# Optimization experiments

Hardware: AMD Instinct MI355X
Metric: run time of the kernel (lower is better)

## Reference

```python
import jax, jax.numpy as jnp
import numpy as np

B, T, C, H = 8, 2048, 1024, 128  # batch, seq (=block_size), n_embd, head_size


def setup_inputs() -> dict:
    key = jax.random.key(0)
    kx, kk, kq, kv = jax.random.split(key, 4)
    x = jax.random.normal(kx, (B, T, C), dtype=jnp.float32)
    # nn.Linear(n_embd, head_size, bias=False) weights, stored as (in, out) for x @ W
    s = 1.0 / np.sqrt(C)
    Wk = jax.random.normal(kk, (C, H), dtype=jnp.float32) * s
    Wq = jax.random.normal(kq, (C, H), dtype=jnp.float32) * s
    Wv = jax.random.normal(kv, (C, H), dtype=jnp.float32) * s
    return {"x": x, "Wk": Wk, "Wq": Wq, "Wv": Wv}


def reference(x, Wk, Wq, Wv):
    # x: [B, T, C]
    Bx, Tx, Cx = x.shape
    k = x @ Wk  # [B, T, H]
    q = x @ Wq  # [B, T, H]
    v = x @ Wv  # [B, T, H]
    # NOTE: source multiplies by C**0.5 (not 1/sqrt), kept faithfully
    wei = jnp.einsum("bth,bsh->bts", q, k) * (Cx ** 0.5)  # [B, T, T]
    causal = jnp.tril(jnp.ones((Tx, Tx), dtype=bool))
    wei = jnp.where(causal, wei, -jnp.inf)
    wei = jax.nn.softmax(wei, axis=-1)
    # dropout omitted (eval-mode reference)
    return wei @ v  # [B, T, H]
```

## Files before the change

### kernel.cpp

```cpp
#include <hip/hip_runtime.h>

constexpr int kB = 8;
constexpr int kT = 2048;
constexpr int kC = 1024;
constexpr int kH = 128;
constexpr int kM = kB * kT;
constexpr size_t kMH = (size_t)kM * kH;
constexpr size_t kWH = (size_t)kC * kH;

#define QSCALE 46.166241308446828f

typedef __attribute__((ext_vector_type(8))) short bf16x8;
typedef __attribute__((ext_vector_type(4))) float f32x4;


__device__ inline unsigned short f2bf_rne(float f) {
    union { float f; unsigned int u; } x; x.f = f;
    unsigned int r = x.u + 0x7fff + ((x.u >> 16) & 1);
    return (unsigned short)(r >> 16);
}
__device__ inline float bf2f(unsigned short h) {
    union { float f; unsigned int u; } x; x.u = ((unsigned int)h) << 16;
    return x.f;
}
__device__ inline unsigned int pack_hi2(float a, float b) {
    return __builtin_amdgcn_perm(__float_as_uint(b), __float_as_uint(a),
                                 0x07060302u);
}
__device__ inline float hi_part(float v) {
    return __uint_as_float(__float_as_uint(v) & 0xffff0000u);
}
__device__ inline void load_lds16(const unsigned short* g, unsigned short* l) {
    __builtin_amdgcn_global_load_lds(
        (const __attribute__((address_space(1))) unsigned int*)g,
        (__attribute__((address_space(3))) unsigned int*)l, 16, 0, 0);
}

template <int CTRL>
__device__ inline float dpp_rot(float x) {
    return __int_as_float(__builtin_amdgcn_update_dpp(
        0, __float_as_int(x), CTRL, 0xf, 0xf, false));
}
__device__ inline float rowmax16(float x) {
    x = fmaxf(x, dpp_rot<0x121>(x));
    x = fmaxf(x, dpp_rot<0x122>(x));
    x = fmaxf(x, dpp_rot<0x124>(x));
    x = fmaxf(x, dpp_rot<0x128>(x));
    return x;
}
__device__ inline float rowsum16(float x) {
    x += dpp_rot<0x121>(x);
    x += dpp_rot<0x122>(x);
    x += dpp_rot<0x124>(x);
    x += dpp_rot<0x128>(x);
    return x;
}

__global__ __launch_bounds__(256) void prep_w(
    const float* __restrict__ Wk, const float* __restrict__ Wq,
    const float* __restrict__ Wv, unsigned short* __restrict__ ws)
{
    const int h = blockIdx.x;
    const int mat = blockIdx.y;
    const float* W = (mat == 0) ? Wq : (mat == 1) ? Wk : Wv;
    unsigned short* hi = ws + 5 * kMH + (size_t)(mat * 2) * kWH;
    unsigned short* lo = hi + kWH;

    const int k0 = threadIdx.x * 4;
    unsigned short hv[4], lv[4];
#pragma unroll
    for (int j = 0; j < 4; ++j) {
        const float f = W[(size_t)(k0 + j) * kH + h];
        hv[j] = f2bf_rne(f);
        lv[j] = f2bf_rne(f - bf2f(hv[j]));
    }
    *(uint2*)&hi[(size_t)h * kC + k0] =
        make_uint2(((unsigned)hv[1] << 16) | hv[0], ((unsigned)hv[3] << 16) | hv[2]);
    *(uint2*)&lo[(size_t)h * kC + k0] =
        make_uint2(((unsigned)lv[1] << 16) | lv[0], ((unsigned)lv[3] << 16) | lv[2]);
}

__global__ __launch_bounds__(256) void qkv_mfma(
    const float* __restrict__ x, unsigned short* __restrict__ ws)
{
    __shared__ __align__(16) unsigned short Bh[128 * 64];
    __shared__ __align__(16) unsigned short Bl[128 * 64];

    const int idx = blockIdx.x;
    const int mat = idx >> 8;
    const int m0 = (idx & 255) * 64;
    const unsigned short* wThi = ws + 5 * kMH + (size_t)(mat * 2) * kWH;
    const unsigned short* wTlo = wThi + kWH;

    const int tid = threadIdx.x;
    const int w = tid >> 6, lane = tid & 63;
    const int li = lane & 15, quad = lane >> 4;

    const float* xrow = x + (size_t)(m0 + w * 16 + li) * kC;

    f32x4 acc[8];
#pragma unroll
    for (int j = 0; j < 8; ++j) acc[j] = (f32x4){0.f, 0.f, 0.f, 0.f};

    for (int kt = 0; kt < kC; kt += 64) {
        if (kt) __syncthreads();
#pragma unroll
        for (int u = 0; u < 4; ++u) {
            const int f = u * 256 + tid;
            const int row = f >> 3, g = (f & 7) ^ (row & 7);
            load_lds16(wThi + (size_t)row * kC + kt + g * 8, Bh + f * 8);
            if (mat <= 1)
                load_lds16(wTlo + (size_t)row * kC + kt + g * 8, Bl + f * 8);
        }
        float4 xa[2][2];
#pragma unroll
        for (int kc = 0; kc < 2; ++kc) {
            xa[kc][0] = *(const float4*)(xrow + kt + kc * 32 + quad * 8);
            xa[kc][1] = *(const float4*)(xrow + kt + kc * 32 + quad * 8 + 4);
        }
        bf16x8 ah[2], al[2];
        if (mat <= 1) {
#pragma unroll
            for (int kc = 0; kc < 2; ++kc) {
                const float4 a0 = xa[kc][0], a1 = xa[kc][1];
                unsigned int hp[4], lp[4];
                hp[0] = pack_hi2(a0.x, a0.y); hp[1] = pack_hi2(a0.z, a0.w);
                hp[2] = pack_hi2(a1.x, a1.y); hp[3] = pack_hi2(a1.z, a1.w);
                lp[0] = pack_hi2(a0.x - hi_part(a0.x), a0.y - hi_part(a0.y));
                lp[1] = pack_hi2(a0.z - hi_part(a0.z), a0.w - hi_part(a0.w));
                lp[2] = pack_hi2(a1.x - hi_part(a1.x), a1.y - hi_part(a1.y));
                lp[3] = pack_hi2(a1.z - hi_part(a1.z), a1.w - hi_part(a1.w));
                ah[kc] = *(bf16x8*)hp;
                al[kc] = *(bf16x8*)lp;
            }
        } else {
#pragma unroll
            for (int kc = 0; kc < 2; ++kc) {
                const float4 a0 = xa[kc][0], a1 = xa[kc][1];
                unsigned short e[8];
                e[0] = f2bf_rne(a0.x); e[1] = f2bf_rne(a0.y);
                e[2] = f2bf_rne(a0.z); e[3] = f2bf_rne(a0.w);
                e[4] = f2bf_rne(a1.x); e[5] = f2bf_rne(a1.y);
                e[6] = f2bf_rne(a1.z); e[7] = f2bf_rne(a1.w);
                ah[kc] = *(bf16x8*)e;
            }
        }
        __syncthreads();

        if (mat <= 1) {
#pragma unroll
            for (int kc = 0; kc < 2; ++kc)
#pragma unroll
                for (int nt = 0; nt < 8; ++nt) {
                    const int row = nt * 16 + li;
                    const int pos = (kc * 4 + quad) ^ (row & 7);
                    const bf16x8 bh = *(const bf16x8*)&Bh[row * 64 + pos * 8];
                    const bf16x8 bl = *(const bf16x8*)&Bl[row * 64 + pos * 8];
                    acc[nt] = __builtin_amdgcn_mfma_f32_16x16x32_bf16(ah[kc], bh, acc[nt], 0, 0, 0);
                    acc[nt] = __builtin_amdgcn_mfma_f32_16x16x32_bf16(al[kc], bh, acc[nt], 0, 0, 0);
                    acc[nt] = __builtin_amdgcn_mfma_f32_16x16x32_bf16(ah[kc], bl, acc[nt], 0, 0, 0);
                }
        } else {
#pragma unroll
            for (int kc = 0; kc < 2; ++kc)
#pragma unroll
                for (int nt = 0; nt < 8; ++nt) {
                    const int row = nt * 16 + li;
                    const int pos = (kc * 4 + quad) ^ (row & 7);
                    const bf16x8 bh = *(const bf16x8*)&Bh[row * 64 + pos * 8];
                    acc[nt] = __builtin_amdgcn_mfma_f32_16x16x32_bf16(ah[kc], bh, acc[nt], 0, 0, 0);
                }
        }
    }

    if (mat <= 1) {
        unsigned short* hip_ = ws + (size_t)(mat * 2) * kMH;
        unsigned short* lop  = hip_ + kMH;
        const float sc = (mat == 0) ? QSCALE : 1.0f;
#pragma unroll
        for (int nt = 0; nt < 8; ++nt) {
            const int col = nt * 16 + li;
#pragma unroll
            for (int reg = 0; reg < 4; ++reg) {
                const int row = m0 + w * 16 + quad * 4 + reg;
                const float v = acc[nt][reg] * sc;
                hip_[(size_t)row * kH + col] = (unsigned short)(__float_as_uint(v) >> 16);
                lop[(size_t)row * kH + col] =
                    (unsigned short)(__float_as_uint(v - hi_part(v)) >> 16);
            }
        }
    } else {
        unsigned short* vt = ws + 4 * kMH;
        const int bb = m0 >> 11;
        const int t0 = (m0 & (kT - 1)) + w * 16 + quad * 4;
#pragma unroll
        for (int nt = 0; nt < 8; ++nt) {
            const int h = nt * 16 + li;
            ushort4 pk;
            pk.x = f2bf_rne(acc[nt][0]);
            pk.y = f2bf_rne(acc[nt][1]);
            pk.z = f2bf_rne(acc[nt][2]);
            pk.w = f2bf_rne(acc[nt][3]);
            *(ushort4*)&vt[((size_t)(bb * kH + h)) * kT + t0] = pk;
        }
    }
}

__global__ __launch_bounds__(256, 2) void attn_mfma(
    const unsigned short* __restrict__ ws, float* __restrict__ out)
{
    __shared__ __align__(16) unsigned short Ps[4][2][16][40];
    __shared__ __align__(16) float Ml[4][32][2];
    __shared__ __align__(16) float Obuf[3][32][128];

    const int tid = threadIdx.x;
    const int w = tid >> 6, lane = tid & 63;
    const int li = lane & 15, quad = lane >> 4;

    const int idx = blockIdx.x;
    const int b = idx & 7;
    const int j = idx >> 3;
    const int qt = (j < 32) ? j : 95 - j;
    const int i0 = qt * 32;
    const int nc = qt + 1;

    const unsigned short* qhi = ws;
    const unsigned short* qlo = ws + kMH;
    const unsigned short* khi = ws + 2 * kMH;
    const unsigned short* klo = ws + 3 * kMH;
    const unsigned short* vt  = ws + 4 * kMH;

    bf16x8 qh[2][4], ql[2][4];
#pragma unroll
    for (int mi = 0; mi < 2; ++mi) {
        const size_t qoff = ((size_t)(b * kT + i0 + mi * 16 + li)) * kH;
#pragma unroll
        for (int kc = 0; kc < 4; ++kc) {
            qh[mi][kc] = *(const bf16x8*)(qhi + qoff + kc * 32 + quad * 8);
            ql[mi][kc] = *(const bf16x8*)(qlo + qoff + kc * 32 + quad * 8);
        }
    }

    f32x4 o[2][8];
#pragma unroll
    for (int mi = 0; mi < 2; ++mi)
#pragma unroll
        for (int ht = 0; ht < 8; ++ht) o[mi][ht] = (f32x4){0.f, 0.f, 0.f, 0.f};
    float m_i[2][4], l_i[2][4];
#pragma unroll
    for (int mi = 0; mi < 2; ++mi)
#pragma unroll
        for (int reg = 0; reg < 4; ++reg) { m_i[mi][reg] = -3.0e38f; l_i[mi][reg] = 0.f; }

    for (int jc = w; jc < nc; jc += 4) {
        const int t0 = jc * 32;
        bf16x8 vf[8];
#pragma unroll
        for (int ht = 0; ht < 8; ++ht)
            vf[ht] = *(const bf16x8*)(vt + (size_t)(b * kH + ht * 16 + li) * kT +
                                      t0 + quad * 8);
        f32x4 s[2][2];
#pragma unroll
        for (int mi = 0; mi < 2; ++mi)
#pragma unroll
            for (int nt = 0; nt < 2; ++nt) s[mi][nt] = (f32x4){0.f, 0.f, 0.f, 0.f};
#pragma unroll
        for (int kc = 0; kc < 4; ++kc) {
            bf16x8 kh[2], kl[2];
#pragma unroll
            for (int nt = 0; nt < 2; ++nt) {
                const size_t ka =
                    ((size_t)(b * kT + t0 + nt * 16 + li)) * kH + kc * 32 + quad * 8;
                kh[nt] = *(const bf16x8*)(khi + ka);
                kl[nt] = *(const bf16x8*)(klo + ka);
            }
#pragma unroll
            for (int mi = 0; mi < 2; ++mi)
#pragma unroll
                for (int nt = 0; nt < 2; ++nt) {
                    s[mi][nt] = __builtin_amdgcn_mfma_f32_16x16x32_bf16(qh[mi][kc], kh[nt], s[mi][nt], 0, 0, 0);
                    s[mi][nt] = __builtin_amdgcn_mfma_f32_16x16x32_bf16(ql[mi][kc], kh[nt], s[mi][nt], 0, 0, 0);
                    s[mi][nt] = __builtin_amdgcn_mfma_f32_16x16x32_bf16(qh[mi][kc], kl[nt], s[mi][nt], 0, 0, 0);
                }
        }
        if (jc == qt) {
#pragma unroll
            for (int mi = 0; mi < 2; ++mi) {
                const int grow0 = i0 + mi * 16 + quad * 4;
#pragma unroll
                for (int nt = 0; nt < 2; ++nt) {
                    const int gcol = t0 + nt * 16 + li;
#pragma unroll
                    for (int reg = 0; reg < 4; ++reg)
                        if (gcol > grow0 + reg) s[mi][nt][reg] = -3.0e38f;
                }
            }
        }
#pragma unroll
        for (int mi = 0; mi < 2; ++mi) {
            float alpha[4];
#pragma unroll
            for (int reg = 0; reg < 4; ++reg) {
                const float mr = rowmax16(fmaxf(s[mi][0][reg], s[mi][1][reg]));
                const float mn = fmaxf(m_i[mi][reg], mr);
                alpha[reg] = exp2f(m_i[mi][reg] - mn);
                m_i[mi][reg] = mn;
                const float p0 = exp2f(s[mi][0][reg] - mn);
                const float p1 = exp2f(s[mi][1][reg] - mn);
                s[mi][0][reg] = p0; s[mi][1][reg] = p1;
                const float rs = rowsum16(p0 + p1);
                l_i[mi][reg] = l_i[mi][reg] * alpha[reg] + rs;
            }
            const f32x4 av = {alpha[0], alpha[1], alpha[2], alpha[3]};
#pragma unroll
            for (int ht = 0; ht < 8; ++ht) o[mi][ht] *= av;
#pragma unroll
            for (int nt = 0; nt < 2; ++nt)
#pragma unroll
                for (int reg = 0; reg < 4; ++reg)
                    Ps[w][mi][quad * 4 + reg][nt * 16 + li] = f2bf_rne(s[mi][nt][reg]);
        }
#pragma unroll
        for (int mi = 0; mi < 2; ++mi) {
            const bf16x8 pf = *(const bf16x8*)&Ps[w][mi][li][quad * 8];
#pragma unroll
            for (int ht = 0; ht < 8; ++ht)
                o[mi][ht] = __builtin_amdgcn_mfma_f32_16x16x32_bf16(pf, vf[ht], o[mi][ht], 0, 0, 0);
        }
    }

    if (li == 0) {
#pragma unroll
        for (int mi = 0; mi < 2; ++mi)
#pragma unroll
            for (int reg = 0; reg < 4; ++reg) {
                Ml[w][mi * 16 + quad * 4 + reg][0] = m_i[mi][reg];
                Ml[w][mi * 16 + quad * 4 + reg][1] = l_i[mi][reg];
            }
    }
    __syncthreads();
    float a_self[2][4], linv[2][4];
#pragma unroll
    for (int mi = 0; mi < 2; ++mi)
#pragma unroll
        for (int reg = 0; reg < 4; ++reg) {
            const int row = mi * 16 + quad * 4 + reg;
            const float m0_ = Ml[0][row][0], m1 = Ml[1][row][0];
            const float m2 = Ml[2][row][0], m3 = Ml[3][row][0];
            const float ms = fmaxf(fmaxf(m0_, m1), fmaxf(m2, m3));
            const float L = Ml[0][row][1] * exp2f(m0_ - ms) +
                            Ml[1][row][1] * exp2f(m1 - ms) +
                            Ml[2][row][1] * exp2f(m2 - ms) +
                            Ml[3][row][1] * exp2f(m3 - ms);
            a_self[mi][reg] = exp2f(m_i[mi][reg] - ms);
            linv[mi][reg] = 1.0f / L;
        }
    if (w) {
#pragma unroll
        for (int mi = 0; mi < 2; ++mi)
#pragma unroll
            for (int ht = 0; ht < 8; ++ht)
#pragma unroll
                for (int reg = 0; reg < 4; ++reg)
                    Obuf[w - 1][mi * 16 + quad * 4 + reg][ht * 16 + li] =
                        o[mi][ht][reg] * a_self[mi][reg];
    }
    __syncthreads();
    if (w == 0) {
#pragma unroll
        for (int mi = 0; mi < 2; ++mi)
#pragma unroll
            for (int ht = 0; ht < 8; ++ht)
#pragma unroll
                for (int reg = 0; reg < 4; ++reg) {
                    const int row = mi * 16 + quad * 4 + reg;
                    const int col = ht * 16 + li;
                    const float v = o[mi][ht][reg] * a_self[mi][reg] +
                                    Obuf[0][row][col] + Obuf[1][row][col] +
                                    Obuf[2][row][col];
                    out[(size_t)(b * kT + i0 + row) * kH + col] = v * linv[mi][reg];
                }
    }
}

extern "C" void kernel_launch(void* const* d_in, const int* in_sizes, int n_in,
                              void* d_out, int out_size, void* d_ws, size_t ws_size,
                              hipStream_t stream) {
    const float* x  = (const float*)d_in[0];
    const float* Wk = (const float*)d_in[1];
    const float* Wq = (const float*)d_in[2];
    const float* Wv = (const float*)d_in[3];
    unsigned short* ws = (unsigned short*)d_ws;
    float* out = (float*)d_out;

    hipLaunchKernelGGL(prep_w, dim3(128, 3), dim3(256), 0, stream, Wk, Wq, Wv, ws);
    hipLaunchKernelGGL(qkv_mfma, dim3(768), dim3(256), 0, stream, x, ws);
    hipLaunchKernelGGL(attn_mfma, dim3(512), dim3(256), 0, stream,
                       (const unsigned short*)ws, out);
}
```

Baseline: 190.0 us.

## Store Q/K/V projections in MFMA-fragment-tiled layout for contiguous wave loads

The projection kernel now writes Q/K hi/lo and V^T into a pre-swizzled layout in which each 64-lane MFMA operand fragment is a contiguous 1 KB block. The attention kernel then loads Q, K and V fragments with lane*8 offsets, giving fully coalesced 16-byte-per-lane reads instead of strided row accesses. This cuts the memory transactions per fragment in the bandwidth-heavy attention loop. In exchange the projection stores become more scattered, and both kernels must agree exactly on the index math.

Result: no change. 193.0 us (+1.6%).

```diff
diff --git a/kernel.cpp b/kernel.cpp
--- a/kernel.cpp
+++ b/kernel.cpp
@@ -173,35 +173,41 @@
         }
     }
 
+    const int bb = m0 >> 11;
     if (mat <= 1) {
         unsigned short* hip_ = ws + (size_t)(mat * 2) * kMH;
         unsigned short* lop  = hip_ + kMH;
         const float sc = (mat == 0) ? QSCALE : 1.0f;
+        const int tb = ((m0 & 2047) >> 4) + w;
 #pragma unroll
         for (int nt = 0; nt < 8; ++nt) {
-            const int col = nt * 16 + li;
+            const int kc = nt >> 1;
+            const int lup = ((nt & 1) << 1) | (li >> 3);
+            const int jj = li & 7;
+            const size_t fb =
+                ((((size_t)bb * 128 + tb) * 4 + kc) * 64 + (lup << 4) + quad * 4) * 8 + jj;
 #pragma unroll
             for (int reg = 0; reg < 4; ++reg) {
-                const int row = m0 + w * 16 + quad * 4 + reg;
                 const float v = acc[nt][reg] * sc;
-                hip_[(size_t)row * kH + col] = (unsigned short)(__float_as_uint(v) >> 16);
-                lop[(size_t)row * kH + col] =
+                hip_[fb + (size_t)reg * 8] = (unsigned short)(__float_as_uint(v) >> 16);
+                lop[fb + (size_t)reg * 8] =
                     (unsigned short)(__float_as_uint(v - hi_part(v)) >> 16);
             }
         }
     } else {
         unsigned short* vt = ws + 4 * kMH;
-        const int bb = m0 >> 11;
-        const int t0 = (m0 & (kT - 1)) + w * 16 + quad * 4;
+        const int jc = ((m0 & 2047) >> 5) + (w >> 1);
+        const int lup = ((w & 1) << 1) | (quad >> 1);
+        const int j0 = (quad & 1) * 4;
 #pragma unroll
         for (int nt = 0; nt < 8; ++nt) {
-            const int h = nt * 16 + li;
             ushort4 pk;
             pk.x = f2bf_rne(acc[nt][0]);
             pk.y = f2bf_rne(acc[nt][1]);
             pk.z = f2bf_rne(acc[nt][2]);
             pk.w = f2bf_rne(acc[nt][3]);
-            *(ushort4*)&vt[((size_t)(bb * kH + h)) * kT + t0] = pk;
+            *(ushort4*)&vt[(((((size_t)bb * 64 + jc) * 8 + nt) * 64) +
+                            (lup << 4) + li) * 8 + j0] = pk;
         }
     }
 }
@@ -233,11 +239,11 @@
     bf16x8 qh[2][4], ql[2][4];
 #pragma unroll
     for (int mi = 0; mi < 2; ++mi) {
-        const size_t qoff = ((size_t)(b * kT + i0 + mi * 16 + li)) * kH;
+        const size_t qb = (((size_t)b * 128 + qt * 2 + mi) * 4) * 512 + lane * 8;
 #pragma unroll
         for (int kc = 0; kc < 4; ++kc) {
-            qh[mi][kc] = *(const bf16x8*)(qhi + qoff + kc * 32 + quad * 8);
-            ql[mi][kc] = *(const bf16x8*)(qlo + qoff + kc * 32 + quad * 8);
+            qh[mi][kc] = *(const bf16x8*)(qhi + qb + kc * 512);
+            ql[mi][kc] = *(const bf16x8*)(qlo + qb + kc * 512);
         }
     }
 
@@ -254,11 +260,12 @@
 
     for (int jc = w; jc < nc; jc += 4) {
         const int t0 = jc * 32;
+        const size_t vbb = (((size_t)b * 64 + jc) * 8) * 512 + lane * 8;
         bf16x8 vf[8];
 #pragma unroll
         for (int ht = 0; ht < 8; ++ht)
-            vf[ht] = *(const bf16x8*)(vt + (size_t)(b * kH + ht * 16 + li) * kT +
-                                      t0 + quad * 8);
+            vf[ht] = *(const bf16x8*)(vt + vbb + ht * 512);
+        const size_t kbb = (((size_t)b * 128 + jc * 2) * 4) * 512 + lane * 8;
         f32x4 s[2][2];
 #pragma unroll
         for (int mi = 0; mi < 2; ++mi)
@@ -269,8 +276,7 @@
             bf16x8 kh[2], kl[2];
 #pragma unroll
             for (int nt = 0; nt < 2; ++nt) {
-                const size_t ka =
-                    ((size_t)(b * kT + t0 + nt * 16 + li)) * kH + kc * 32 + quad * 8;
+                const size_t ka = kbb + (nt * 4 + kc) * 512;
                 kh[nt] = *(const bf16x8*)(khi + ka);
                 kl[nt] = *(const bf16x8*)(klo + ka);
             }
```
